# Optimization experiments

Measured on AMD Instinct MI355X. Metric: run time of the kernel, lower is better.

## Reference

```python
import jax, jax.numpy as jnp
import numpy as np

D_MODEL = 1024
NUM_TILES = 64
TPC = 8                      # tiles_per_cluster
NUM_CLUSTERS = NUM_TILES // TPC
GRID = 16
COMP_H = 256                 # compress hidden = d_model // 4
NUM_KNOTS = 8
EPS_LN = 1e-5


def setup_inputs() -> dict:
    key = jax.random.key(0)
    ks = jax.random.split(key, 12)
    B, T = 4, 4096
    x = jax.random.normal(ks[0], (B, T, D_MODEL), dtype=jnp.float32)
    signatures_raw = jax.random.normal(ks[1], (NUM_TILES, D_MODEL), dtype=jnp.float32) * 0.5
    knot_values = jax.nn.sigmoid(jnp.linspace(-3.0, 3.0, NUM_KNOTS).astype(jnp.float32))
    temperature = jnp.ones((1,), dtype=jnp.float32)
    # compress: Linear(d,comp_h) -> GELU -> Linear(comp_h,2) -> Tanh
    compress_w1 = jax.random.normal(ks[2], (D_MODEL, COMP_H), dtype=jnp.float32) * (1.0 / np.sqrt(D_MODEL))
    compress_b1 = jnp.zeros((COMP_H,), dtype=jnp.float32)
    compress_w2 = jax.random.normal(ks[3], (COMP_H, 2), dtype=jnp.float32) * (1.0 / np.sqrt(COMP_H))
    compress_b2 = jnp.zeros((2,), dtype=jnp.float32)
    # per-tile magnitude splines: Linear(2,grid) -> ReLU -> Linear(grid,1)
    spline_w1 = jax.random.normal(ks[4], (NUM_TILES, 2, GRID), dtype=jnp.float32) * (1.0 / np.sqrt(2.0))
    spline_b1 = jnp.zeros((NUM_TILES, GRID), dtype=jnp.float32)
    spline_w2 = jax.random.normal(ks[5], (NUM_TILES, GRID, 1), dtype=jnp.float32) * (1.0 / np.sqrt(GRID))
    spline_b2 = jnp.zeros((NUM_TILES, 1), dtype=jnp.float32)
    directions = jax.random.normal(ks[6], (NUM_TILES, D_MODEL), dtype=jnp.float32) * 0.02
    norm_gamma = jnp.ones((D_MODEL,), dtype=jnp.float32)
    norm_beta = jnp.zeros((D_MODEL,), dtype=jnp.float32)
    output_scale = jnp.ones((1,), dtype=jnp.float32) * 0.1
    return dict(x=x, signatures_raw=signatures_raw, knot_values=knot_values,
                temperature=temperature, compress_w1=compress_w1, compress_b1=compress_b1,
                compress_w2=compress_w2, compress_b2=compress_b2, spline_w1=spline_w1,
                spline_b1=spline_b1, spline_w2=spline_w2, spline_b2=spline_b2,
                directions=directions, norm_gamma=norm_gamma, norm_beta=norm_beta,
                output_scale=output_scale)


def _calibrate(scores, knots, temperature):
    # ScoreCalibrationSpline: sigmoid -> linear interpolation over knots
    K = knots.shape[0]
    normalized = jax.nn.sigmoid(scores / (temperature[0] + 1e-6))
    idx_float = normalized * (K - 1)
    idx_low = jnp.clip(idx_float.astype(jnp.int32), 0, K - 2)
    idx_high = idx_low + 1
    t = idx_float - idx_low.astype(scores.dtype)
    val_low = knots[idx_low]
    val_high = knots[idx_high]
    return val_low + t * (val_high - val_low)


def _forward(x, signatures_raw, knot_values, temperature, compress_w1, compress_b1,
             compress_w2, compress_b2, spline_w1, spline_b1, spline_w2, spline_b2,
             directions, norm_gamma, norm_beta, output_scale):
    B, T, D = x.shape
    xf = x.reshape(-1, D)  # [N, D]

    # ternary quantized signatures with straight-through estimator
    q = jnp.where(signatures_raw > 0.3, 1.0,
                  jnp.where(signatures_raw < -0.3, -1.0, 0.0)).astype(signatures_raw.dtype)
    sigs = signatures_raw + jax.lax.stop_gradient(q - signatures_raw)  # [NT, D]

    # hierarchical routing: cluster signatures = sign(mean of member sigs)
    cluster_sigs = jnp.sign(sigs.reshape(NUM_CLUSTERS, TPC, D).mean(axis=1))  # [NC, D]
    cluster_scores = xf @ cluster_sigs.T                                       # [N, NC]
    cluster_gates = _calibrate(cluster_scores, knot_values, temperature)
    cluster_idx = jnp.argmax(cluster_gates, axis=-1)                           # [N]

    # within-cluster tile selection (clusters are contiguous blocks of tiles)
    tile_scores = xf @ sigs.T                                                  # [N, NT]
    tile_gates = _calibrate(tile_scores, knot_values, temperature)
    gates_by_cluster = tile_gates.reshape(-1, NUM_CLUSTERS, TPC)
    sel_gates = jnp.take_along_axis(gates_by_cluster, cluster_idx[:, None, None],
                                    axis=1)[:, 0, :]                            # [N, TPC]
    local_idx = jnp.argmax(sel_gates, axis=-1)
    tile_idx = cluster_idx * TPC + local_idx                                    # [N]

    # compress to 2D spline coordinates
    h = jax.nn.gelu(xf @ compress_w1 + compress_b1, approximate=False)
    comp = jnp.tanh(h @ compress_w2 + compress_b2)                              # [N, 2]

    # batched per-token tiny spline MLP (gather selected tile's weights)
    w1 = spline_w1[tile_idx]                                                    # [N, 2, G]
    b1 = spline_b1[tile_idx]                                                    # [N, G]
    hh = jax.nn.relu(jnp.einsum('ni,nig->ng', comp, w1) + b1)                   # [N, G]
    w2 = spline_w2[tile_idx]                                                    # [N, G, 1]
    b2 = spline_b2[tile_idx]                                                    # [N, 1]
    mag = jnp.einsum('ng,ngo->no', hh, w2) + b2                                 # [N, 1]

    ffn_out = mag * directions[tile_idx] * output_scale[0]                      # [N, D]

    # residual + LayerNorm (dropout in eval mode = identity)
    y = xf + ffn_out
    mu = y.mean(axis=-1, keepdims=True)
    var = ((y - mu) ** 2).mean(axis=-1, keepdims=True)
    y = (y - mu) / jnp.sqrt(var + EPS_LN) * norm_gamma + norm_beta
    return y.reshape(B, T, D)


def reference(x, signatures_raw, knot_values, temperature, compress_w1, compress_b1,
              compress_w2, compress_b2, spline_w1, spline_b1, spline_w2, spline_b2,
              directions, norm_gamma, norm_beta, output_scale):
    return _forward(x, signatures_raw, knot_values, temperature, compress_w1, compress_b1,
                    compress_w2, compress_b2, spline_w1, spline_b1, spline_w2, spline_b2,
                    directions, norm_gamma, norm_beta, output_scale)
```

## Files before the change

### kernel.cpp

```cpp
#include <hip/hip_runtime.h>
#include <hip/hip_bf16.h>
#include <cmath>

#define N_TOK 16384
#define DM    1024
#define CH    256
#define SGRID 16
#define NTP   24

typedef __attribute__((ext_vector_type(8))) short short8;
typedef __attribute__((ext_vector_type(4))) float floatx4;

__device__ __forceinline__ unsigned short f2bf(float f) {
  union { float f; unsigned int u; } v; v.f = f;
  unsigned int r = v.u + 0x7FFFu + ((v.u >> 16) & 1u);
  return (unsigned short)(r >> 16);
}

__device__ __forceinline__ short8 cvt8(float4 u, float4 v) {
  union { short8 s; __hip_bfloat162 h[4]; } r;
  r.h[0] = __float22bfloat162_rn(make_float2(u.x, u.y));
  r.h[1] = __float22bfloat162_rn(make_float2(u.z, u.w));
  r.h[2] = __float22bfloat162_rn(make_float2(v.x, v.y));
  r.h[3] = __float22bfloat162_rn(make_float2(v.z, v.w));
  return r.s;
}

__device__ __forceinline__ float bf2f(unsigned short b) {
  union { unsigned int u; float f; } v; v.u = ((unsigned int)b) << 16; return v.f;
}

__device__ __forceinline__ float calibrate(float s, const float* __restrict__ kn, float temp_eff) {
  float nrm = 1.0f / (1.0f + expf(-s / temp_eff));
  float idxf = nrm * 7.0f;
  int il = (int)idxf; if (il > 6) il = 6;
  float tt = idxf - (float)il;
  float lo = kn[il], hi = kn[il + 1];
  return lo + tt * (hi - lo);
}

__global__ __launch_bounds__(256) void prep_kernel(
    const float* __restrict__ sig_raw, const float* __restrict__ w1,
    unsigned short* __restrict__ wsB) {
  __shared__ float Wt[32][260];
  __shared__ float St[64][33];
  int kk = blockIdx.x, tid = threadIdx.x;
  {
    int r = tid >> 3, c0 = (tid & 7) * 32;
    const float* src = w1 + (size_t)(kk * 32 + r) * CH + c0;
#pragma unroll
    for (int i = 0; i < 8; ++i)
      *(float4*)(&Wt[r][c0 + 4 * i]) = *(const float4*)(src + 4 * i);
  }
  {
    int t = tid >> 2, c0 = (tid & 3) * 8;
    const float* src = sig_raw + (size_t)t * DM + kk * 32 + c0;
#pragma unroll
    for (int i = 0; i < 8; ++i) {
      float rr = src[i];
      St[t][c0 + i] = (rr > 0.3f) ? 1.f : ((rr < -0.3f) ? -1.f : 0.f);
    }
  }
  __syncthreads();
#pragma unroll
  for (int i = 0; i < 4; ++i) {
    int idx = i * 256 + tid;
    int nt = idx >> 6, lane = idx & 63;
    int q = lane >> 4, l = lane & 15;
    short8 v;
#pragma unroll
    for (int j = 0; j < 8; ++j) v[j] = (short)f2bf(Wt[q * 8 + j][nt * 16 + l]);
    *(short8*)(wsB + ((size_t)(kk * NTP + nt) * 64 + lane) * 8) = v;
  }
#pragma unroll
  for (int i = 0; i < 2; ++i) {
    int idx = i * 256 + tid;
    if (idx < 320) {
      int nt = 16 + (idx >> 6), lane = idx & 63;
      int q = lane >> 4, l = lane & 15;
      int n = nt * 16 + l;
      short8 v;
#pragma unroll
      for (int j = 0; j < 8; ++j) {
        int kl = q * 8 + j;
        float val = 0.f;
        if (n < 264) {
          float s = 0.f;
#pragma unroll
          for (int m = 0; m < 8; ++m) s += St[(n - 256) * 8 + m][kl];
          val = (s > 0.f) ? 1.f : ((s < 0.f) ? -1.f : 0.f);
        } else if (n < 328) {
          val = St[n - 264][kl];
        }
        v[j] = (short)f2bf(val);
      }
      *(short8*)(wsB + ((size_t)(kk * NTP + nt) * 64 + lane) * 8) = v;
    }
  }
}


#define LOADK(kk, b0, b1, av)                                               \
  {                                                                         \
    const char* bp = bBase + (size_t)(kk) * (NTP * 1024);                   \
    b0 = *(const short8*)(bp);                                              \
    if (wave < 5) b1 = *(const short8*)(bp + 16384);                        \
    unsigned cpos = ((unsigned)((kk) * 4 + quad) ^ sw) << 3;                \
    _Pragma("unroll") for (int mt = 0; mt < 4; ++mt)                        \
        av[mt] = *(const short8*)(Xsh + mt * 16384 + arow + cpos);          \
  }

#define COMPUTE(b0, b1, av)                                                 \
  {                                                                         \
    _Pragma("unroll") for (int mt = 0; mt < 4; ++mt)                        \
      acc0[mt] = __builtin_amdgcn_mfma_f32_16x16x32_bf16(av[mt], b0, acc0[mt], 0, 0, 0); \
    if (wave < 5) {                                                         \
      _Pragma("unroll") for (int mt = 0; mt < 4; ++mt)                      \
        acc1[mt] = __builtin_amdgcn_mfma_f32_16x16x32_bf16(av[mt], b1, acc1[mt], 0, 0, 0); \
    }                                                                       \
  }

__global__ __launch_bounds__(1024, 4) void fused_kernel(
    const float* __restrict__ x, const unsigned short* __restrict__ wsB,
    const float* __restrict__ b1v, const float* __restrict__ w2,
    const float* __restrict__ b2, const float* __restrict__ knots,
    const float* __restrict__ temperature, const float* __restrict__ sw1,
    const float* __restrict__ sb1, const float* __restrict__ sw2,
    const float* __restrict__ sb2, const float* __restrict__ dirs,
    const float* __restrict__ gma, const float* __restrict__ bta,
    const float* __restrict__ oscale, float* __restrict__ out) {
  __shared__ unsigned short Xsh[64 * 1024];
  __shared__ float Ssc[64][73];
  __shared__ float Psh[16][64][2];
  __shared__ float ScaleS[64];
  __shared__ int   TidxS[64];

  int tid = threadIdx.x;
  int wave = tid >> 6, lane = tid & 63, quad = lane >> 4, l15 = lane & 15;
  int m0 = blockIdx.x * 64;

  {
    const float* base = x + (size_t)m0 * DM;
#pragma unroll
    for (int i2 = 0; i2 < 8; ++i2) {
      int cg = tid + 1024 * i2;
      float4 p = *(const float4*)(base + cg * 8);
      float4 q = *(const float4*)(base + cg * 8 + 4);
      int row = cg >> 7, cir = cg & 127;
      int pos = cir ^ (row & 7);
      *(short8*)(Xsh + row * 1024 + pos * 8) = cvt8(p, q);
    }
  }
  __syncthreads();

  floatx4 acc0[4], acc1[4];
#pragma unroll
  for (int mt = 0; mt < 4; ++mt) {
    acc0[mt] = (floatx4){0.f, 0.f, 0.f, 0.f};
    acc1[mt] = (floatx4){0.f, 0.f, 0.f, 0.f};
  }

  const char* bBase = (const char*)wsB + wave * 1024 + lane * 16;
  int arow = l15 * 1024;
  unsigned sw = (unsigned)(l15 & 7);

  short8 bA0, bA1, bB0, bB1, aA[4], aB_[4];
  LOADK(0, bA0, bA1, aA);
#pragma unroll 1
  for (int kk = 0; kk < 30; kk += 2) {
    LOADK(kk + 1, bB0, bB1, aB_);
    COMPUTE(bA0, bA1, aA);
    LOADK(kk + 2, bA0, bA1, aA);
    COMPUTE(bB0, bB1, aB_);
  }
  LOADK(31, bB0, bB1, aB_);
  COMPUTE(bA0, bA1, aA);
  COMPUTE(bB0, bB1, aB_);

  if (wave < 5) {
    int sc = wave * 16 + l15;
    if (sc < 72) {
#pragma unroll
      for (int mt = 0; mt < 4; ++mt)
#pragma unroll
        for (int r = 0; r < 4; ++r)
          Ssc[mt * 16 + quad * 4 + r][sc] = acc1[mt][r];
    }
  }

  {
    int col = wave * 16 + l15;
    float b1c = b1v[col], w20 = w2[2 * col], w21 = w2[2 * col + 1];
    float p0[4], p1[4];
#pragma unroll
    for (int mt = 0; mt < 4; ++mt) { p0[mt] = 0.f; p1[mt] = 0.f; }
#pragma unroll
    for (int mt = 0; mt < 4; ++mt)
#pragma unroll
      for (int r = 0; r < 4; ++r) {
        float hh = acc0[mt][r] + b1c;
        hh = 0.5f * hh * (1.0f + erff(hh * 0.7071067811865475f));
        if (r == 0) { p0[mt] += hh * w20; p1[mt] += hh * w21; }
        else if (r == 1) { p0[mt] = p0[mt]; p1[mt] = p1[mt]; p0[mt] += 0.f; p1[mt] += 0.f;
        }
      }
  }
  {
    int col = wave * 16 + l15;
    float b1c = b1v[col], w20 = w2[2 * col], w21 = w2[2 * col + 1];
    float q0[4][4], q1[4][4];
#pragma unroll
    for (int mt = 0; mt < 4; ++mt)
#pragma unroll
      for (int r = 0; r < 4; ++r) {
        float hh = acc0[mt][r] + b1c;
        hh = 0.5f * hh * (1.0f + erff(hh * 0.7071067811865475f));
        q0[mt][r] = hh * w20;
        q1[mt][r] = hh * w21;
      }
#pragma unroll
    for (int m = 1; m < 16; m <<= 1)
#pragma unroll
      for (int mt = 0; mt < 4; ++mt)
#pragma unroll
        for (int r = 0; r < 4; ++r) {
          q0[mt][r] += __shfl_xor(q0[mt][r], m);
          q1[mt][r] += __shfl_xor(q1[mt][r], m);
        }
    if (l15 == 0) {
#pragma unroll
      for (int mt = 0; mt < 4; ++mt)
#pragma unroll
        for (int r = 0; r < 4; ++r) {
          Psh[wave][mt * 16 + quad * 4 + r][0] = q0[mt][r];
          Psh[wave][mt * 16 + quad * 4 + r][1] = q1[mt][r];
        }
    }
  }
  __syncthreads();

  if (tid < 64) {
    int row = tid;
    float s0 = b2[0], s1 = b2[1];
#pragma unroll
    for (int j = 0; j < 16; ++j) {
      s0 += Psh[j][row][0];
      s1 += Psh[j][row][1];
    }
    float c0 = tanhf(s0), c1 = tanhf(s1);

    float temp_eff = temperature[0] + 1e-6f;
    int cid = 0; float best = -1e30f;
#pragma unroll
    for (int c = 0; c < 8; ++c) {
      float g = calibrate(Ssc[row][c], knots, temp_eff);
      if (g > best) { best = g; cid = c; }
    }
    int lidx = 0; best = -1e30f;
#pragma unroll
    for (int j = 0; j < 8; ++j) {
      float g = calibrate(Ssc[row][8 + cid * 8 + j], knots, temp_eff);
      if (g > best) { best = g; lidx = j; }
    }
    int t = cid * 8 + lidx;

    float mag = sb2[t];
#pragma unroll
    for (int g2 = 0; g2 < SGRID; ++g2) {
      float hv = c0 * sw1[t * 32 + g2] + c1 * sw1[t * 32 + 16 + g2] + sb1[t * 16 + g2];
      hv = fmaxf(hv, 0.f);
      mag += hv * sw2[t * 16 + g2];
    }
    ScaleS[row] = mag * oscale[0];
    TidxS[row] = t;
  }
  __syncthreads();

#pragma unroll 1
  for (int rr = 0; rr < 4; ++rr) {
    int row = wave * 4 + rr;
    int r7 = row & 7;
    float scale = ScaleS[row];
    const float* dr = dirs + (size_t)TidxS[row] * DM + lane * 16;
    const unsigned short* xrow = Xsh + row * 1024;
    short8 h0 = *(const short8*)(xrow + (unsigned)((2 * lane) ^ r7) * 8);
    short8 h1 = *(const short8*)(xrow + (unsigned)((2 * lane + 1) ^ r7) * 8);
    float fv[16];
    float ssum = 0.f, ssq = 0.f;
#pragma unroll
    for (int i = 0; i < 4; ++i) {
      float4 d4 = *(const float4*)(dr + 4 * i);
      float xa = bf2f((unsigned short)((i < 2 ? h0[i * 4 + 0] : h1[(i - 2) * 4 + 0])));
      float xb = bf2f((unsigned short)((i < 2 ? h0[i * 4 + 1] : h1[(i - 2) * 4 + 1])));
      float xc = bf2f((unsigned short)((i < 2 ? h0[i * 4 + 2] : h1[(i - 2) * 4 + 2])));
      float xd = bf2f((unsigned short)((i < 2 ? h0[i * 4 + 3] : h1[(i - 2) * 4 + 3])));
      fv[4 * i + 0] = xa + scale * d4.x;
      fv[4 * i + 1] = xb + scale * d4.y;
      fv[4 * i + 2] = xc + scale * d4.z;
      fv[4 * i + 3] = xd + scale * d4.w;
      ssum += fv[4 * i + 0] + fv[4 * i + 1] + fv[4 * i + 2] + fv[4 * i + 3];
      ssq += fv[4 * i + 0] * fv[4 * i + 0] + fv[4 * i + 1] * fv[4 * i + 1]
           + fv[4 * i + 2] * fv[4 * i + 2] + fv[4 * i + 3] * fv[4 * i + 3];
    }
#pragma unroll
    for (int m = 1; m < 64; m <<= 1) {
      ssum += __shfl_xor(ssum, m);
      ssq += __shfl_xor(ssq, m);
    }
    float mu = ssum * (1.0f / 1024.0f);
    float var = ssq * (1.0f / 1024.0f) - mu * mu;
    float inv = rsqrtf(var + 1e-5f);
    float* orow = out + (size_t)(m0 + row) * DM + lane * 16;
    const float* gp = gma + lane * 16;
    const float* bp2 = bta + lane * 16;
#pragma unroll
    for (int i = 0; i < 4; ++i) {
      float4 g4 = *(const float4*)(gp + 4 * i);
      float4 b4 = *(const float4*)(bp2 + 4 * i);
      float4 o;
      o.x = (fv[4 * i + 0] - mu) * inv * g4.x + b4.x;
      o.y = (fv[4 * i + 1] - mu) * inv * g4.y + b4.y;
      o.z = (fv[4 * i + 2] - mu) * inv * g4.z + b4.z;
      o.w = (fv[4 * i + 3] - mu) * inv * g4.w + b4.w;
      *(float4*)(orow + 4 * i) = o;
    }
  }
}

extern "C" void kernel_launch(void* const* d_in, const int* in_sizes, int n_in,
                              void* d_out, int out_size, void* d_ws, size_t ws_size,
                              hipStream_t stream) {
  const float* x      = (const float*)d_in[0];
  const float* sigraw = (const float*)d_in[1];
  const float* knots  = (const float*)d_in[2];
  const float* temp   = (const float*)d_in[3];
  const float* cw1    = (const float*)d_in[4];
  const float* cb1    = (const float*)d_in[5];
  const float* cw2    = (const float*)d_in[6];
  const float* cb2    = (const float*)d_in[7];
  const float* sw1    = (const float*)d_in[8];
  const float* sb1    = (const float*)d_in[9];
  const float* sw2    = (const float*)d_in[10];
  const float* sb2    = (const float*)d_in[11];
  const float* dirs   = (const float*)d_in[12];
  const float* gma    = (const float*)d_in[13];
  const float* bta    = (const float*)d_in[14];
  const float* oscale = (const float*)d_in[15];
  float* out = (float*)d_out;

  unsigned short* wsB = (unsigned short*)d_ws;

  hipLaunchKernelGGL(prep_kernel, dim3(32), dim3(256), 0, stream,
                     sigraw, cw1, wsB);
  hipLaunchKernelGGL(fused_kernel, dim3(N_TOK / 64), dim3(1024), 0, stream,
                     x, wsB, cb1, cw2, cb2, knots, temp,
                     sw1, sb1, sw2, sb2, dirs, gma, bta, oscale, out);
}
```

Baseline: 176.1 us.

## Pipeline x tile staging into shared memory across K-stages with MFMA compute

Replaces the single up-front load of the whole 64x1024 x tile into LDS with four 256-column stages. The global loads for the next stage are issued before the MFMA loop over the current stage and written to LDS after it, with a barrier per stage. The aim is to hide global-memory latency behind matrix work when only about one large block fits per CU. It also drops a dead GELU block whose results were never used. The cost is three extra block-wide barriers and more live registers for the staged float4 values.

```diff
diff --git a/kernel.cpp b/kernel.cpp
--- a/kernel.cpp
+++ b/kernel.cpp
@@ -118,6 +118,22 @@
       _Pragma("unroll") for (int mt = 0; mt < 4; ++mt)                      \
         acc1[mt] = __builtin_amdgcn_mfma_f32_16x16x32_bf16(av[mt], b1, acc1[mt], 0, 0, 0); \
     }                                                                       \
+  }
+
+#define STAGE_LOAD(s)                                                       \
+  {                                                                         \
+    const float* p0 = xbase + row0 * 1024 + (32 * (s) + ci0) * 8;           \
+    lA[0] = ((const float4*)p0)[0];                                         \
+    lA[1] = ((const float4*)p0)[1];                                         \
+    const float* p1 = xbase + row1 * 1024 + (32 * (s) + ci1) * 8;           \
+    lA[2] = ((const float4*)p1)[0];                                         \
+    lA[3] = ((const float4*)p1)[1];                                         \
+  }
+
+#define STAGE_WRITE(s)                                                      \
+  {                                                                         \
+    *(short8*)(Xsh + row0 * 1024 + ((unsigned)((32 * (s) + ci0) ^ (row0 & 7))) * 8) = cvt8(lA[0], lA[1]); \
+    *(short8*)(Xsh + row1 * 1024 + ((unsigned)((32 * (s) + ci1) ^ (row1 & 7))) * 8) = cvt8(lA[2], lA[3]); \
   }
 
 __global__ __launch_bounds__(1024, 4) void fused_kernel(
@@ -139,19 +155,9 @@
   int wave = tid >> 6, lane = tid & 63, quad = lane >> 4, l15 = lane & 15;
   int m0 = blockIdx.x * 64;
 
-  {
-    const float* base = x + (size_t)m0 * DM;
-#pragma unroll
-    for (int i2 = 0; i2 < 8; ++i2) {
-      int cg = tid + 1024 * i2;
-      float4 p = *(const float4*)(base + cg * 8);
-      float4 q = *(const float4*)(base + cg * 8 + 4);
-      int row = cg >> 7, cir = cg & 127;
-      int pos = cir ^ (row & 7);
-      *(short8*)(Xsh + row * 1024 + pos * 8) = cvt8(p, q);
-    }
-  }
-  __syncthreads();
+  const float* xbase = x + (size_t)m0 * DM;
+  int row0 = tid >> 5, ci0 = tid & 31;
+  int row1 = row0 + 32, ci1 = ci0;
 
   floatx4 acc0[4], acc1[4];
 #pragma unroll
@@ -164,18 +170,30 @@
   int arow = l15 * 1024;
   unsigned sw = (unsigned)(l15 & 7);
 
+  float4 lA[4];
+  STAGE_LOAD(0);
+  STAGE_WRITE(0);
+  __syncthreads();
+
   short8 bA0, bA1, bB0, bB1, aA[4], aB_[4];
-  LOADK(0, bA0, bA1, aA);
 #pragma unroll 1
-  for (int kk = 0; kk < 30; kk += 2) {
-    LOADK(kk + 1, bB0, bB1, aB_);
+  for (int s = 0; s < 4; ++s) {
+    if (s < 3) STAGE_LOAD(s + 1);
+    int k0 = 8 * s;
+    LOADK(k0, bA0, bA1, aA);
+#pragma unroll
+    for (int j = 0; j < 3; ++j) {
+      LOADK(k0 + 2 * j + 1, bB0, bB1, aB_);
+      COMPUTE(bA0, bA1, aA);
+      LOADK(k0 + 2 * j + 2, bA0, bA1, aA);
+      COMPUTE(bB0, bB1, aB_);
+    }
+    LOADK(k0 + 7, bB0, bB1, aB_);
     COMPUTE(bA0, bA1, aA);
-    LOADK(kk + 2, bA0, bA1, aA);
     COMPUTE(bB0, bB1, aB_);
-  }
-  LOADK(31, bB0, bB1, aB_);
-  COMPUTE(bA0, bA1, aA);
-  COMPUTE(bB0, bB1, aB_);
+    if (s < 3) STAGE_WRITE(s + 1);
+    __syncthreads();
+  }
 
   if (wave < 5) {
     int sc = wave * 16 + l15;
@@ -188,23 +206,6 @@
     }
   }
 
-  {
-    int col = wave * 16 + l15;
-    float b1c = b1v[col], w20 = w2[2 * col], w21 = w2[2 * col + 1];
-    float p0[4], p1[4];
-#pragma unroll
-    for (int mt = 0; mt < 4; ++mt) { p0[mt] = 0.f; p1[mt] = 0.f; }
-#pragma unroll
-    for (int mt = 0; mt < 4; ++mt)
-#pragma unroll
-      for (int r = 0; r < 4; ++r) {
-        float hh = acc0[mt][r] + b1c;
-        hh = 0.5f * hh * (1.0f + erff(hh * 0.7071067811865475f));
-        if (r == 0) { p0[mt] += hh * w20; p1[mt] += hh * w21; }
-        else if (r == 1) { p0[mt] = p0[mt]; p1[mt] = p1[mt]; p0[mt] += 0.f; p1[mt] += 0.f;
-        }
-      }
-  }
   {
     int col = wave * 16 + l15;
     float b1c = b1v[col], w20 = w2[2 * col], w21 = w2[2 * col + 1];
```

After: 178.4 us. Within noise of the previous version (+1.3%).
